# Optimization experiments

Hardware: AMD Instinct MI355X
Metric: run time of the kernel (lower is better)

## Reference

```python
import jax, jax.numpy as jnp
import numpy as np

NORM_EPS = 1e-6
QK_SCALE = 1.0 / 128.0  # 1/d_head (muP)
ROTARY_BASE = 10000
INFTY_APPROX = 1e30

B, T, M, H, D = 2, 2048, 1024, 8, 128


def _rmsnorm(x, eps=NORM_EPS):
    # normalize over the last (head) dim; no learned gains (norm_gains=False)
    ms = jnp.mean(jnp.square(x), axis=-1, keepdims=True)
    return x / jnp.sqrt(ms + eps)


def _rope(x, base=ROTARY_BASE):
    # x: [b, h, t, d]; rotate (even-half, odd-half) pairs as in the source
    length, width = x.shape[-2], x.shape[-1]
    half = width // 2
    pos = jnp.arange(length, dtype=x.dtype)[:, None]            # [t, 1]
    freqs = jnp.power(jnp.asarray(base, x.dtype), -jnp.arange(half, dtype=x.dtype) / half)[None, :]
    rad = pos * freqs                                            # [t, half]
    cos = jnp.cos(rad)[None, None]
    sin = jnp.sin(rad)[None, None]
    even, odd = jnp.split(x, 2, axis=-1)
    return jnp.concatenate([even * cos - odd * sin, even * sin + odd * cos], axis=-1)


def setup_inputs() -> dict:
    key = jax.random.key(0)
    ks = jax.random.split(key, 5)
    std = M ** -0.5
    return {
        "x": jax.random.normal(ks[0], (B, T, M), jnp.float32),
        "wq": jax.random.normal(ks[1], (M, H, D), jnp.float32) * std,
        "wk": jax.random.normal(ks[2], (M, H, D), jnp.float32) * std,
        "wv": jax.random.normal(ks[3], (M, H, D), jnp.float32) * std,
        "wo": jax.random.normal(ks[4], (H, D, M), jnp.float32) * std,
    }


def reference(x, wq, wk, wv, wo):
    # projections: [b, h, t, d]
    q = jnp.einsum('bim,mhd->bhid', x, wq)
    k = jnp.einsum('bim,mhd->bhid', x, wk)
    v = jnp.einsum('bim,mhd->bhid', x, wv)
    # qk RMSNorm (norm_gains=False)
    q = _rmsnorm(q)
    k = _rmsnorm(k)
    # inline RoPE
    q = _rope(q)
    k = _rope(k)
    # scaled scores: mult applied to both q and k (mult^2 = qk_scale)
    mult = jnp.asarray(QK_SCALE ** 0.5, q.dtype)
    s = jnp.einsum('bhid,bhjd->bhij', q * mult, k * mult)
    # causal mask: subtract large constant where i < j
    t = s.shape[-1]
    mask = (jnp.arange(t)[:, None] < jnp.arange(t)[None, :]).astype(s.dtype)
    s = s - jnp.asarray(INFTY_APPROX, s.dtype) * mask[None, None]
    p = jax.nn.softmax(s, axis=-1)
    o = jnp.einsum('bhij,bhjd->bhid', p, v)
    return jnp.einsum('bhid,hdm->bim', o, wo)
```

## Files before the change

### kernel.cpp

```cpp
#include <hip/hip_runtime.h>
#include <hip/hip_bf16.h>
#include <math.h>

#define B_  2
#define T_  2048
#define M_  1024
#define H_  8
#define D_  128
#define NROW (B_ * T_)
#define HD  (H_ * D_)

#define NORM_EPS 1e-6f
#define QK_MULT  0.08838834764831845f
#define ROT_BASE 10000.0f

typedef short bf16x8  __attribute__((ext_vector_type(8)));
typedef float f32x4   __attribute__((ext_vector_type(4)));
typedef float f32x16  __attribute__((ext_vector_type(16)));

static __device__ __forceinline__ unsigned short f2bf(float f) {
    union { __hip_bfloat16 h; unsigned short u; } cv;
    cv.h = __float2bfloat16(f);
    return cv.u;
}
static __device__ __forceinline__ float bf2f(unsigned short u) {
    union { unsigned short u; __hip_bfloat16 h; } cv;
    cv.u = u;
    return __bfloat162float(cv.h);
}
static __device__ __forceinline__ unsigned int pk2bf(float a, float b) {
    return ((unsigned int)f2bf(b) << 16) | f2bf(a);
}

static __device__ __forceinline__ void gload_lds16(const unsigned short* g,
                                                   unsigned short* l) {
    __builtin_amdgcn_global_load_lds(
        (const __attribute__((address_space(1))) void*)g,
        (__attribute__((address_space(3))) void*)l, 16, 0, 0);
}

__global__ __launch_bounds__(256) void cast_bf16(const float* __restrict__ in,
                                                 unsigned short* __restrict__ out)
{
    const int i = (blockIdx.x * 256 + threadIdx.x) * 4;
    const float4 v = *(const float4*)(in + i);
    ushort4 o;
    o.x = f2bf(v.x); o.y = f2bf(v.y); o.z = f2bf(v.z); o.w = f2bf(v.w);
    *(ushort4*)(out + i) = o;
}

__global__ __launch_bounds__(256) void transpose_cast4(const float* __restrict__ w0,
                                                       const float* __restrict__ w1,
                                                       const float* __restrict__ w2,
                                                       const float* __restrict__ w3,
                                                       unsigned short* __restrict__ wqkvT,
                                                       unsigned short* __restrict__ woT)
{
    __shared__ float t[32][33];
    const int z = blockIdx.z;
    const float* in = z == 0 ? w0 : (z == 1 ? w1 : (z == 2 ? w2 : w3));
    unsigned short* out = z < 3 ? (wqkvT + (size_t)z * 1024 * 1024) : woT;

    const int tx = threadIdx.x & 31;
    const int ty = threadIdx.x >> 5;
    const int n0 = blockIdx.x * 32;
    const int k0 = blockIdx.y * 32;
    #pragma unroll
    for (int r = 0; r < 4; ++r)
        t[ty + r * 8][tx] = in[(size_t)(k0 + ty + r * 8) * 1024 + n0 + tx];
    __syncthreads();
    #pragma unroll
    for (int r = 0; r < 4; ++r)
        out[(size_t)(n0 + ty + r * 8) * 1024 + k0 + tx] = f2bf(t[tx][ty + r * 8]);
}

template <int MODE>
__global__ __launch_bounds__(256) void gemm_bt(const unsigned short* __restrict__ A,
                                               const unsigned short* __restrict__ Bt,
                                               unsigned short* __restrict__ oq,
                                               unsigned short* __restrict__ ok,
                                               unsigned short* __restrict__ vt,
                                               float* __restrict__ cf)
{
    __shared__ unsigned short As[128 * 32];
    __shared__ unsigned short Bs[128 * 32];

    const int tid  = threadIdx.x;
    const int lane = tid & 63;
    const int w    = tid >> 6;
    const int g    = lane >> 4;
    const int lc   = lane & 15;
    const int wm   = w >> 1;
    const int wn   = w & 1;

    const int m0 = blockIdx.y * 128;
    const int n0 = blockIdx.x * 128;

    const unsigned short* aBase = A  + (size_t)m0 * 1024;
    const unsigned short* bBase = Bt + (size_t)n0 * 1024;

    f32x4 acc[4][4];
    #pragma unroll
    for (int i = 0; i < 4; ++i)
        #pragma unroll
        for (int j = 0; j < 4; ++j)
            acc[i][j] = (f32x4){0.f, 0.f, 0.f, 0.f};

    for (int kt = 0; kt < 32; ++kt) {
        const int k0 = kt * 32;
        #pragma unroll
        for (int it = 0; it < 2; ++it) {
            const int u  = tid + it * 256;
            const int r2 = u >> 2;
            const int s2 = u & 3;
            gload_lds16(aBase + (size_t)r2 * 1024 + k0 + s2 * 8, &As[u * 8]);
            gload_lds16(bBase + (size_t)r2 * 1024 + k0 + s2 * 8, &Bs[u * 8]);
        }
        __syncthreads();

        bf16x8 af[4], bfr[4];
        #pragma unroll
        for (int i = 0; i < 4; ++i)
            af[i] = *(const bf16x8*)&As[(wm * 64 + i * 16 + lc) * 32 + g * 8];
        #pragma unroll
        for (int j = 0; j < 4; ++j)
            bfr[j] = *(const bf16x8*)&Bs[(wn * 64 + j * 16 + lc) * 32 + g * 8];

        #pragma unroll
        for (int i = 0; i < 4; ++i)
            #pragma unroll
            for (int j = 0; j < 4; ++j)
                acc[i][j] = __builtin_amdgcn_mfma_f32_16x16x32_bf16(af[i], bfr[j], acc[i][j], 0, 0, 0);
        __syncthreads();
    }

    if (MODE == 0) {
        const int which = n0 >> 10;
        const int ncol0 = (n0 & 1023) + wn * 64;
        if (which < 2) {
            unsigned short* outp = which == 0 ? oq : ok;
            #pragma unroll
            for (int i = 0; i < 4; ++i) {
                const int mrow = m0 + wm * 64 + i * 16 + g * 4;
                #pragma unroll
                for (int j = 0; j < 4; ++j) {
                    const int nc = ncol0 + j * 16 + lc;
                    #pragma unroll
                    for (int r = 0; r < 4; ++r)
                        outp[(size_t)(mrow + r) * 1024 + nc] = f2bf(acc[i][j][r]);
                }
            }
        } else {
            const int b2 = m0 >> 11;
            #pragma unroll
            for (int i = 0; i < 4; ++i) {
                const int t = (m0 & 2047) + wm * 64 + i * 16 + g * 4;
                #pragma unroll
                for (int j = 0; j < 4; ++j) {
                    const int nc = ncol0 + j * 16 + lc;
                    const int hh = nc >> 7, dd = nc & 127;
                    uint2 val;
                    val.x = pk2bf(acc[i][j][0], acc[i][j][1]);
                    val.y = pk2bf(acc[i][j][2], acc[i][j][3]);
                    *(uint2*)(vt + (((size_t)(b2 * 8 + hh) * 128 + dd) * T_ + t)) = val;
                }
            }
        }
    } else {
        #pragma unroll
        for (int i = 0; i < 4; ++i) {
            const int mrow = m0 + wm * 64 + i * 16 + g * 4;
            #pragma unroll
            for (int j = 0; j < 4; ++j) {
                const int nc = n0 + wn * 64 + j * 16 + lc;
                #pragma unroll
                for (int r = 0; r < 4; ++r)
                    cf[(size_t)(mrow + r) * 1024 + nc] = acc[i][j][r];
            }
        }
    }
}

__global__ __launch_bounds__(256) void rmsnorm_rope_bf16(unsigned short* __restrict__ q,
                                                         unsigned short* __restrict__ k)
{
    const int vec = blockIdx.x * 4 + (threadIdx.x >> 6);
    unsigned short* p = (blockIdx.y == 0 ? q : k) + (size_t)vec * 128;
    const int t = (vec / H_) % T_;
    const int lane = threadIdx.x & 63;

    float e = bf2f(p[lane]);
    float o = bf2f(p[lane + 64]);
    float ss = e * e + o * o;
    #pragma unroll
    for (int off = 32; off; off >>= 1) ss += __shfl_xor(ss, off);
    const float r = rsqrtf(ss * (1.0f / 128.0f) + NORM_EPS) * QK_MULT;
    e *= r;
    o *= r;

    const float freq = expf(-(float)lane * (logf(ROT_BASE) / 64.0f));
    const float rad = (float)t * freq;
    const float c = cosf(rad);
    const float s = sinf(rad);

    p[lane]      = f2bf(e * c - o * s);
    p[lane + 64] = f2bf(e * s + o * c);
}

__global__ __launch_bounds__(256) void flash_attn(const unsigned short* __restrict__ qb,
                                                  const unsigned short* __restrict__ kb,
                                                  const unsigned short* __restrict__ vt,
                                                  unsigned short* __restrict__ o)
{
    __shared__ __align__(16) unsigned short smem[2 * 64 * 128 + 2 * 128 * 64 + 128];
    unsigned short* KsB = smem;
    unsigned short* VsB = smem + 2 * 64 * 128;
    float* lscr = (float*)(smem + 2 * 64 * 128 + 2 * 128 * 64);
    float* scr  = (float*)smem;

    const int tid  = threadIdx.x;
    const int lane = tid & 63;
    const int w    = tid >> 6;
    const int wj   = w >> 1;
    const int wq2  = w & 1;
    const int qcol = lane & 31;
    const int hi   = lane >> 5;

    const int bh = blockIdx.x;
    const int h  = bh & (H_ - 1);
    const int b  = bh >> 3;
    const int yy = blockIdx.y;
    const int qt = (yy & 1) ? (31 - (yy >> 1)) : (yy >> 1);
    const int q0 = qt * 64;

    const size_t bhbase  = (size_t)b * T_ * HD + (size_t)h * 128;
    const size_t bhvbase = (size_t)bh * 128 * T_;

    int mI[4];
    size_t srcKoff[4], srcVoff[4];
    #pragma unroll
    for (int it = 0; it < 4; ++it) {
        const int m = (w * 4 + it) * 64 + lane;
        mI[it] = m;
        const int jK = m >> 4, cK = (m & 15) ^ (jK & 15);
        srcKoff[it] = (size_t)jK * 1024 + cK * 8;
        const int dV = m >> 3, cV = (m & 7) ^ (dV & 7);
        srcVoff[it] = (size_t)dV * T_ + cV * 8;
    }
    const unsigned short* kgb = kb + bhbase;
    const unsigned short* vgb = vt + bhvbase;

    bf16x8 qf[8];
    {
        const unsigned short* qp = qb + bhbase + (size_t)(q0 + wq2 * 32 + qcol) * 1024 + hi * 8;
        #pragma unroll
        for (int ks = 0; ks < 8; ++ks)
            qf[ks] = *(const bf16x8*)(qp + ks * 16);
    }

    float lsum = 0.f;
    f32x16 otacc[4];
    #pragma unroll
    for (int dch = 0; dch < 4; ++dch)
        #pragma unroll
        for (int r = 0; r < 16; ++r) otacc[dch][r] = 0.f;

    #pragma unroll
    for (int it = 0; it < 4; ++it) {
        gload_lds16(kgb + srcKoff[it], &KsB[mI[it] * 8]);
        gload_lds16(vgb + srcVoff[it], &VsB[mI[it] * 8]);
    }

    for (int jt = 0; jt <= qt; ++jt) {
        const int cur = jt & 1;
        unsigned short* Ks = KsB + cur * (64 * 128);
        unsigned short* Vs = VsB + cur * (128 * 64);
        __syncthreads();

        if (jt < qt) {
            const size_t j0n = (size_t)(jt + 1) * 64;
            unsigned short* Kn = KsB + (cur ^ 1) * (64 * 128);
            unsigned short* Vn = VsB + (cur ^ 1) * (128 * 64);
            #pragma unroll
            for (int it = 0; it < 4; ++it) {
                gload_lds16(kgb + j0n * 1024 + srcKoff[it], &Kn[mI[it] * 8]);
                gload_lds16(vgb + j0n + srcVoff[it], &Vn[mI[it] * 8]);
            }
        }

        const bool dead = (jt == qt) && (wj > wq2);
        if (!dead) {
            f32x16 sacc;
            #pragma unroll
            for (int r = 0; r < 16; ++r) sacc[r] = 0.f;
            const int jrow = wj * 32 + qcol;
            #pragma unroll
            for (int ks = 0; ks < 8; ++ks) {
                const int c = ks * 2 + hi;
                bf16x8 af = *(const bf16x8*)&Ks[(jrow * 16 + (c ^ (lane & 15))) * 8];
                sacc = __builtin_amdgcn_mfma_f32_32x32x16_bf16(af, qf[ks], sacc, 0, 0, 0);
            }

            if (jt == qt && wj == wq2) {
                #pragma unroll
                for (int r = 0; r < 16; ++r) {
                    const int jl = (r & 3) + 8 * (r >> 2) + 4 * hi;
                    if (qcol < jl) sacc[r] = -1e30f;
                }
            }

            unsigned int dw[8];
            #pragma unroll
            for (int m2 = 0; m2 < 8; ++m2) {
                const float p0 = __expf(sacc[2 * m2]);
                const float p1 = __expf(sacc[2 * m2 + 1]);
                lsum += p0 + p1;
                dw[m2] = pk2bf(p0, p1);
            }
            unsigned int ex[8];
            #pragma unroll
            for (int m2 = 0; m2 < 8; ++m2)
                ex[m2] = (unsigned int)__shfl_xor((int)dw[m2], 32);

            #pragma unroll
            for (int ks2 = 0; ks2 < 2; ++ks2) {
                union { unsigned int u[4]; bf16x8 v; } pf;
                pf.u[0] = hi ? ex[4 * ks2 + 2] : dw[4 * ks2 + 0];
                pf.u[1] = hi ? ex[4 * ks2 + 3] : dw[4 * ks2 + 1];
                pf.u[2] = hi ? dw[4 * ks2 + 2] : ex[4 * ks2 + 0];
                pf.u[3] = hi ? dw[4 * ks2 + 3] : ex[4 * ks2 + 1];
                #pragma unroll
                for (int dch = 0; dch < 4; ++dch) {
                    const int c = wj * 4 + ks2 * 2 + hi;
                    const int drow = dch * 32 + qcol;
                    bf16x8 af = *(const bf16x8*)&Vs[(drow * 8 + (c ^ (lane & 7))) * 8];
                    otacc[dch] = __builtin_amdgcn_mfma_f32_32x32x16_bf16(af, pf.v, otacc[dch], 0, 0, 0);
                }
            }
        }
    }

    lsum += __shfl_xor(lsum, 32);
    __syncthreads();

    if (wj == 1) {
        float* s0 = scr + (size_t)(wq2 * 32 + qcol) * 129;
        #pragma unroll
        for (int dch = 0; dch < 4; ++dch)
            #pragma unroll
            for (int r = 0; r < 16; ++r)
                s0[dch * 32 + (r & 3) + 8 * (r >> 2) + 4 * hi] = otacc[dch][r];
        if (hi == 0) lscr[wq2 * 32 + qcol] = lsum;
    }
    __syncthreads();
    if (wj == 0) {
        const float l = lsum + lscr[wq2 * 32 + qcol];
        const float inv = 1.0f / l;
        const float* s0 = scr + (size_t)(wq2 * 32 + qcol) * 129;
        unsigned short* op = o + bhbase + (size_t)(q0 + wq2 * 32 + qcol) * 1024;
        #pragma unroll
        for (int dch = 0; dch < 4; ++dch) {
            #pragma unroll
            for (int k4 = 0; k4 < 4; ++k4) {
                const int d0 = dch * 32 + 8 * k4 + 4 * hi;
                const float f0 = (otacc[dch][4 * k4 + 0] + s0[d0 + 0]) * inv;
                const float f1 = (otacc[dch][4 * k4 + 1] + s0[d0 + 1]) * inv;
                const float f2 = (otacc[dch][4 * k4 + 2] + s0[d0 + 2]) * inv;
                const float f3 = (otacc[dch][4 * k4 + 3] + s0[d0 + 3]) * inv;
                uint2 val;
                val.x = pk2bf(f0, f1);
                val.y = pk2bf(f2, f3);
                *(uint2*)(op + d0) = val;
            }
        }
    }
}

extern "C" void kernel_launch(void* const* d_in, const int* in_sizes, int n_in,
                              void* d_out, int out_size, void* d_ws, size_t ws_size,
                              hipStream_t stream)
{
    const float* x  = (const float*)d_in[0];
    const float* wq = (const float*)d_in[1];
    const float* wk = (const float*)d_in[2];
    const float* wv = (const float*)d_in[3];
    const float* wo = (const float*)d_in[4];
    float* out = (float*)d_out;

    const size_t SZ = (size_t)NROW * HD;
    unsigned short* qb    = (unsigned short*)d_ws;
    unsigned short* kb    = qb + SZ;
    unsigned short* vt    = kb + SZ;
    unsigned short* ob    = vt + SZ;
    unsigned short* xb    = ob + SZ;
    unsigned short* wqkvT = xb + SZ;
    unsigned short* woT   = wqkvT + 3 * 1024 * 1024;

    cast_bf16<<<SZ / (256 * 4), 256, 0, stream>>>(x, xb);
    transpose_cast4<<<dim3(32, 32, 4), 256, 0, stream>>>(wq, wk, wv, wo, wqkvT, woT);

    gemm_bt<0><<<dim3(24, 32), 256, 0, stream>>>(xb, wqkvT, qb, kb, vt, nullptr);

    rmsnorm_rope_bf16<<<dim3(NROW * H_ / 4, 2), 256, 0, stream>>>(qb, kb);

    flash_attn<<<dim3(B_ * H_, 32), 256, 0, stream>>>(qb, kb, vt, ob);

    gemm_bt<1><<<dim3(8, 32), 256, 0, stream>>>(ob, woT, nullptr, nullptr, nullptr, out);
}
```

Before: 214.6 us.

## Fuse RMSNorm+RoPE into QKV GEMM epilogue and merge cast kernels

Moves the per-head RMSNorm and RoPE into the Q/K epilogue of the QKV projection GEMM. Each 128-column tile spans one head, so the sum of squares is reduced across lanes and the two column-half waves via LDS. The rotation partner is exchanged through an LDS buffer. It also folds the x cast into the weight transpose kernel as an extra grid slice. Together these remove two kernel launches and one read-modify-write pass over q and k, at the cost of a larger LDS footprint, a heavier epilogue, and the rotation partner now being read back as bf16.

```diff
diff --git a/kernel.cpp b/kernel.cpp
--- a/kernel.cpp
+++ b/kernel.cpp
@@ -12,7 +12,7 @@
 
 #define NORM_EPS 1e-6f
 #define QK_MULT  0.08838834764831845f
-#define ROT_BASE 10000.0f
+#define LN_BASE_64 0.14391156510f
 
 typedef short bf16x8  __attribute__((ext_vector_type(8)));
 typedef float f32x4   __attribute__((ext_vector_type(4)));
@@ -39,25 +39,29 @@
         (__attribute__((address_space(3))) void*)l, 16, 0, 0);
 }
 
-__global__ __launch_bounds__(256) void cast_bf16(const float* __restrict__ in,
-                                                 unsigned short* __restrict__ out)
-{
-    const int i = (blockIdx.x * 256 + threadIdx.x) * 4;
-    const float4 v = *(const float4*)(in + i);
-    ushort4 o;
-    o.x = f2bf(v.x); o.y = f2bf(v.y); o.z = f2bf(v.z); o.w = f2bf(v.w);
-    *(ushort4*)(out + i) = o;
-}
-
-__global__ __launch_bounds__(256) void transpose_cast4(const float* __restrict__ w0,
-                                                       const float* __restrict__ w1,
-                                                       const float* __restrict__ w2,
-                                                       const float* __restrict__ w3,
-                                                       unsigned short* __restrict__ wqkvT,
-                                                       unsigned short* __restrict__ woT)
+__global__ __launch_bounds__(256) void prep(const float* __restrict__ x,
+                                            const float* __restrict__ w0,
+                                            const float* __restrict__ w1,
+                                            const float* __restrict__ w2,
+                                            const float* __restrict__ w3,
+                                            unsigned short* __restrict__ xb,
+                                            unsigned short* __restrict__ wqkvT,
+                                            unsigned short* __restrict__ woT)
 {
     __shared__ float t[32][33];
     const int z = blockIdx.z;
+    if (z == 4) {
+        const size_t base = ((size_t)blockIdx.y * 32 + blockIdx.x) * 4096;
+        #pragma unroll
+        for (int it = 0; it < 4; ++it) {
+            const size_t i = base + it * 1024 + threadIdx.x * 4;
+            const float4 v = *(const float4*)(x + i);
+            ushort4 o;
+            o.x = f2bf(v.x); o.y = f2bf(v.y); o.z = f2bf(v.z); o.w = f2bf(v.w);
+            *(ushort4*)(xb + i) = o;
+        }
+        return;
+    }
     const float* in = z == 0 ? w0 : (z == 1 ? w1 : (z == 2 ? w2 : w3));
     unsigned short* out = z < 3 ? (wqkvT + (size_t)z * 1024 * 1024) : woT;
 
@@ -82,8 +86,9 @@
                                                unsigned short* __restrict__ vt,
                                                float* __restrict__ cf)
 {
-    __shared__ unsigned short As[128 * 32];
-    __shared__ unsigned short Bs[128 * 32];
+    __shared__ __align__(16) unsigned short pool[128 * 132 + 512];
+    unsigned short* As = pool;
+    unsigned short* Bs = pool + 128 * 32;
 
     const int tid  = threadIdx.x;
     const int lane = tid & 63;
@@ -139,17 +144,66 @@
         const int ncol0 = (n0 & 1023) + wn * 64;
         if (which < 2) {
             unsigned short* outp = which == 0 ? oq : ok;
-            #pragma unroll
-            for (int i = 0; i < 4; ++i) {
-                const int mrow = m0 + wm * 64 + i * 16 + g * 4;
-                #pragma unroll
-                for (int j = 0; j < 4; ++j) {
-                    const int nc = ncol0 + j * 16 + lc;
+            unsigned short* xbuf = pool;
+            float* sqbuf = (float*)(pool + 128 * 132);
+
+            float sq[4][4];
+            #pragma unroll
+            for (int i = 0; i < 4; ++i)
+                #pragma unroll
+                for (int r = 0; r < 4; ++r) {
+                    float s = acc[i][0][r] * acc[i][0][r] + acc[i][1][r] * acc[i][1][r]
+                            + acc[i][2][r] * acc[i][2][r] + acc[i][3][r] * acc[i][3][r];
+                    #pragma unroll
+                    for (int off = 1; off < 16; off <<= 1) s += __shfl_xor(s, off);
+                    sq[i][r] = s;
+                }
+            if (lc == 0) {
+                #pragma unroll
+                for (int i = 0; i < 4; ++i)
                     #pragma unroll
                     for (int r = 0; r < 4; ++r)
-                        outp[(size_t)(mrow + r) * 1024 + nc] = f2bf(acc[i][j][r]);
-                }
-            }
+                        sqbuf[wn * 128 + wm * 64 + i * 16 + g * 4 + r] = sq[i][r];
+            }
+            __syncthreads();
+
+            #pragma unroll
+            for (int i = 0; i < 4; ++i)
+                #pragma unroll
+                for (int r = 0; r < 4; ++r) {
+                    const int row = wm * 64 + i * 16 + g * 4 + r;
+                    const float tot = sqbuf[row] + sqbuf[128 + row];
+                    const float rms = rsqrtf(tot * (1.0f / 128.0f) + NORM_EPS) * QK_MULT;
+                    #pragma unroll
+                    for (int j = 0; j < 4; ++j) {
+                        acc[i][j][r] *= rms;
+                        xbuf[row * 132 + wn * 64 + j * 16 + lc] = f2bf(acc[i][j][r]);
+                    }
+                }
+            __syncthreads();
+
+            float freq[4];
+            #pragma unroll
+            for (int j = 0; j < 4; ++j)
+                freq[j] = __expf(-(float)(j * 16 + lc) * LN_BASE_64);
+            #pragma unroll
+            for (int i = 0; i < 4; ++i)
+                #pragma unroll
+                for (int r = 0; r < 4; ++r) {
+                    const int row  = wm * 64 + i * 16 + g * 4 + r;
+                    const int trow = m0 + row;
+                    const float tpos = (float)(trow & (T_ - 1));
+                    #pragma unroll
+                    for (int j = 0; j < 4; ++j) {
+                        float sn, cs;
+                        __sincosf(tpos * freq[j], &sn, &cs);
+                        const float own = acc[i][j][r];
+                        const float par = bf2f(xbuf[row * 132 + ((wn ^ 1) * 64) + j * 16 + lc]);
+                        const float outv = (wn == 0) ? (own * cs - par * sn)
+                                                     : (par * sn + own * cs);
+                        outp[(size_t)trow * 1024 + ncol0 + j * 16 + lc] = f2bf(outv);
+                    }
+                }
         } else {
             const int b2 = m0 >> 11;
             #pragma unroll
@@ -179,32 +233,6 @@
             }
         }
     }
-}
-
-__global__ __launch_bounds__(256) void rmsnorm_rope_bf16(unsigned short* __restrict__ q,
-                                                         unsigned short* __restrict__ k)
-{
-    const int vec = blockIdx.x * 4 + (threadIdx.x >> 6);
-    unsigned short* p = (blockIdx.y == 0 ? q : k) + (size_t)vec * 128;
-    const int t = (vec / H_) % T_;
-    const int lane = threadIdx.x & 63;
-
-    float e = bf2f(p[lane]);
-    float o = bf2f(p[lane + 64]);
-    float ss = e * e + o * o;
-    #pragma unroll
-    for (int off = 32; off; off >>= 1) ss += __shfl_xor(ss, off);
-    const float r = rsqrtf(ss * (1.0f / 128.0f) + NORM_EPS) * QK_MULT;
-    e *= r;
-    o *= r;
-
-    const float freq = expf(-(float)lane * (logf(ROT_BASE) / 64.0f));
-    const float rad = (float)t * freq;
-    const float c = cosf(rad);
-    const float s = sinf(rad);
-
-    p[lane]      = f2bf(e * c - o * s);
-    p[lane + 64] = f2bf(e * s + o * c);
 }
 
 __global__ __launch_bounds__(256) void flash_attn(const unsigned short* __restrict__ qb,
@@ -396,13 +424,10 @@
     unsigned short* wqkvT = xb + SZ;
     unsigned short* woT   = wqkvT + 3 * 1024 * 1024;
 
-    cast_bf16<<<SZ / (256 * 4), 256, 0, stream>>>(x, xb);
-    transpose_cast4<<<dim3(32, 32, 4), 256, 0, stream>>>(wq, wk, wv, wo, wqkvT, woT);
+    prep<<<dim3(32, 32, 5), 256, 0, stream>>>(x, wq, wk, wv, wo, xb, wqkvT, woT);
 
     gemm_bt<0><<<dim3(24, 32), 256, 0, stream>>>(xb, wqkvT, qb, kb, vt, nullptr);
 
-    rmsnorm_rope_bf16<<<dim3(NROW * H_ / 4, 2), 256, 0, stream>>>(qb, kb);
-
     flash_attn<<<dim3(B_ * H_, 32), 256, 0, stream>>>(qb, kb, vt, ob);
 
     gemm_bt<1><<<dim3(8, 32), 256, 0, stream>>>(ob, woT, nullptr, nullptr, nullptr, out);
```

Result: faster. 203.7 us (-5.1%).
